# Optimization experiments

Measured on AMD Instinct MI355X. Metric: run time of the kernel, lower is better.

Reference implementation:

```python
import jax, jax.numpy as jnp
import numpy as np
import math

SIM_THRESHOLD = 0.05


def setup_inputs() -> dict:
    key = jax.random.key(0)
    ks = jax.random.split(key, 5)
    B, N, D = 32, 65, 512  # N = seq_len + 1
    gain = 1.0 / math.sqrt(2.0)
    lim = gain * math.sqrt(6.0 / (D + D))  # xavier_uniform with gain 1/sqrt(2)
    c = 1.0 / math.sqrt(D)
    return {
        "desc_embeddings": jax.random.normal(ks[0], (B, N - 1, D), jnp.float32),
        "name_value_embeddings": jax.random.normal(ks[1], (B, N, D), jnp.float32),
        "Wq": jax.random.uniform(ks[2], (D, D), jnp.float32, -lim, lim),
        "bq": jnp.zeros((D,), jnp.float32),
        "Wk": jax.random.uniform(ks[3], (D, D), jnp.float32, -lim, lim),
        "bk": jnp.zeros((D,), jnp.float32),
        "cls": jax.random.uniform(ks[4], (D,), jnp.float32, -c, c),
    }


def reference(desc_embeddings, name_value_embeddings, Wq, bq, Wk, bk, cls):
    # desc_embeddings is accepted but unused, exactly as in the torch module.
    nve = name_value_embeddings
    B, N, D = nve.shape
    S = N - 1

    q = nve @ Wq.T + bq  # [B, N, D]
    k = nve @ Wk.T + bk  # [B, N, D]
    attn = jnp.einsum('bid,bjd->bij', q, k) / math.sqrt(D)  # [B, N, N]

    # no_self_loop: multiplicatively zero the diagonal of the [1:,1:] block (pre-softmax)
    mask = jnp.ones((N, N), attn.dtype).at[1:, 1:].set(1.0 - jnp.eye(S, dtype=attn.dtype))
    attn = jax.nn.softmax(attn * mask, axis=-1)

    # row i's subgraph = {i} U {j : attn[b, i, j] > thr, j >= 1}
    members_all = (attn[:, 1:, 1:] > SIM_THRESHOLD) | jnp.eye(S, dtype=bool)  # [B, S, S]

    # Greedy sequential clustering: row i starts a subgraph only if node i is not
    # already used; its members then get marked used. Implemented with lax.scan
    # carrying the per-batch `used` bitmap (replaces the Python set loop).
    def step(used, xs):
        i, members = xs  # members: [B, S] for row i
        active = ~used[:, i]  # [B] -> is node (i+1) unused, i.e. this row is a leader
        sel = members & active[:, None]
        return used | sel, (active, sel)

    used0 = jnp.zeros((B, S), bool)
    _, (leader, member) = jax.lax.scan(
        step, used0, (jnp.arange(S), members_all.swapaxes(0, 1))
    )
    leader = leader.T.astype(nve.dtype)            # [B, S]
    member = member.transpose(1, 0, 2).astype(nve.dtype)  # [B, S, S]

    # Padded representation of the ragged output: for each leader row i,
    # slot 0 = cls token, slots 1..S = member embeddings (index order == sorted order),
    # zeros elsewhere. (out, leader_mask, member_mask) losslessly encode the
    # original list-of-lists of variable-size subgraphs.
    body = nve[:, None, 1:, :] * member[..., None]        # [B, S, S, D]
    cls_part = leader[:, :, None, None] * cls             # [B, S, 1, D]
    out = jnp.concatenate([cls_part, body], axis=2)       # [B, S, S+1, D]
    return out, leader, member
```

## Files before the change

### kernel.cpp

```cpp
#include <hip/hip_runtime.h>
#include <math.h>

constexpr int B = 32;
constexpr int N = 65;
constexpr int D = 512;
constexpr int S = 64;
constexpr int M = B * N;

constexpr size_t OUT0_ELEMS = (size_t)B * S * (S + 1) * D;
constexpr size_t Q_ELEMS    = (size_t)M * D;
constexpr size_t KT_ELEMS   = (size_t)B * D * N;
constexpr size_t STAGE_BASE = OUT0_ELEMS - Q_ELEMS - KT_ELEMS;
constexpr int ZF4 = (int)(STAGE_BASE / 4);

constexpr int NG_GEMM = 528;
constexpr int NG_FILL = 1536;
constexpr int NC = (B - 1) * S;
constexpr int NA = 1040;
constexpr int NB = 130;

__global__ __launch_bounds__(256) void k1_gemm_fill(
    const float* __restrict__ nve, const float* __restrict__ Wq,
    const float* __restrict__ bq, const float* __restrict__ Wk,
    const float* __restrict__ bk, float* __restrict__ out)
{
    __shared__ float As[32][68];
    __shared__ float Ws[32][68];

    const int gid = blockIdx.x;
    const int tid = threadIdx.x;

    if (gid < NG_GEMM) {
        const int mat = gid >= (NG_GEMM / 2);
        const int t   = mat ? gid - NG_GEMM / 2 : gid;
        const int bm  = (t % 33) * 64;
        const int bn  = (t / 33) * 64;
        const float* W    = mat ? Wk : Wq;
        const float* bias = mat ? bk : bq;

        float* q  = out + STAGE_BASE;
        float* kT = q + Q_ELEMS;

        const int tr = tid / 16;
        const int tc = tid % 16;
        float acc[4][4] = {};

        for (int k0 = 0; k0 < D; k0 += 32) {
            const int r  = tid / 8;
            const int c4 = (tid % 8) * 4;
            #pragma unroll
            for (int p = 0; p < 2; ++p) {
                const int rr = p * 32 + r;
                const int gm = bm + rr;
                float4 v = make_float4(0.f, 0.f, 0.f, 0.f);
                if (gm < M) v = *(const float4*)&nve[(size_t)gm * D + k0 + c4];
                As[c4 + 0][rr] = v.x; As[c4 + 1][rr] = v.y;
                As[c4 + 2][rr] = v.z; As[c4 + 3][rr] = v.w;
                float4 w = *(const float4*)&W[(size_t)(bn + rr) * D + k0 + c4];
                Ws[c4 + 0][rr] = w.x; Ws[c4 + 1][rr] = w.y;
                Ws[c4 + 2][rr] = w.z; Ws[c4 + 3][rr] = w.w;
            }
            __syncthreads();

            #pragma unroll
            for (int kk = 0; kk < 32; ++kk) {
                float a[4], w[4];
                #pragma unroll
                for (int u = 0; u < 4; ++u) a[u] = As[kk][tr * 4 + u];
                #pragma unroll
                for (int u = 0; u < 4; ++u) w[u] = Ws[kk][tc * 4 + u];
                #pragma unroll
                for (int i = 0; i < 4; ++i)
                    #pragma unroll
                    for (int j = 0; j < 4; ++j)
                        acc[i][j] += a[i] * w[j];
            }
            __syncthreads();
        }

        #pragma unroll
        for (int i = 0; i < 4; ++i) {
            const int gm = bm + tr * 4 + i;
            if (gm >= M) continue;
            const int b = gm / N;
            const int n = gm % N;
            if (mat == 0) {
                float4 v;
                v.x = acc[i][0] + bias[bn + tc * 4 + 0];
                v.y = acc[i][1] + bias[bn + tc * 4 + 1];
                v.z = acc[i][2] + bias[bn + tc * 4 + 2];
                v.w = acc[i][3] + bias[bn + tc * 4 + 3];
                *(float4*)&q[(size_t)gm * D + bn + tc * 4] = v;
            } else {
                #pragma unroll
                for (int j = 0; j < 4; ++j) {
                    const int gd = bn + tc * 4 + j;
                    kT[(size_t)b * D * N + (size_t)gd * N + n] = acc[i][j] + bias[gd];
                }
            }
        }
    } else {
        const float4 z = make_float4(0.f, 0.f, 0.f, 0.f);
        float4* o4 = (float4*)out;
        const int nthr = NG_FILL * 256;
        for (int f = (gid - NG_GEMM) * 256 + tid; f < ZF4; f += nthr)
            o4[f] = z;
    }
}

__global__ __launch_bounds__(128) void k2_attn(
    const float* __restrict__ out, unsigned long long* __restrict__ mem)
{
    const float* q  = out + STAGE_BASE;
    const float* kT = q + Q_ELEMS;

    const int bi = blockIdx.x;
    const int b = bi / S;
    const int r = bi % S;
    const int i = r + 1;
    const int t = threadIdx.x;

    __shared__ float qrow[D];
    __shared__ float sc[N];

    *(float4*)&qrow[t * 4] = *(const float4*)&q[((size_t)b * N + i) * D + t * 4];
    __syncthreads();

    if (t < N) {
        const float* kp = &kT[(size_t)b * D * N];
        float acc = 0.f;
        for (int e = 0; e < D; ++e) acc += qrow[e] * kp[(size_t)e * N + t];
        float s = acc * 0.044194173824159216f;
        if (t == i) s = 0.f;
        sc[t] = s;
    }
    __syncthreads();

    if (t < 64) {
        float mx = -INFINITY;
        for (int j = 0; j < N; ++j) mx = fmaxf(mx, sc[j]);
        float sum = 0.f;
        for (int j = 0; j < N; ++j) sum += expf(sc[j] - mx);
        const float p = expf(sc[t + 1] - mx) / sum;
        const bool bit = (p > 0.05f) || (t + 1 == i);
        unsigned long long mask = __ballot(bit);
        if (t == 0) mem[bi] = mask;
    }
}

__global__ void k3_cluster(const unsigned long long* __restrict__ mem,
                           unsigned long long* __restrict__ sel,
                           unsigned long long* __restrict__ lead)
{
    const int b = threadIdx.x;
    if (b >= B) return;
    unsigned long long used = 0ull, lb = 0ull;
    for (int i = 0; i < S; ++i) {
        const unsigned long long row = mem[b * S + i];
        const bool active = !((used >> i) & 1ull);
        const unsigned long long sl = active ? row : 0ull;
        used |= sl;
        lb |= (unsigned long long)active << i;
        sel[b * S + i] = sl;
    }
    lead[b] = lb;
}

__global__ __launch_bounds__(256) void k4_finish(
    const float* __restrict__ nve, const float* __restrict__ cls,
    const unsigned long long* __restrict__ sel,
    const unsigned long long* __restrict__ lead,
    float* __restrict__ out)
{
    const int gid = blockIdx.x;
    const int t = threadIdx.x;

    if (gid < NC) {
        const int b = gid / S;
        const int i = gid % S;
        const unsigned long long lb = lead[b];
        const unsigned long long sb = sel[b * S + i];
        const int h = t >> 7;
        const int tt = t & 127;
        float4* slot0 = (float4*)(out + (((size_t)b * S + i) * (S + 1)) * D);
        for (int s = h; s <= S; s += 2) {
            bool on = (s == 0) ? ((lb >> i) & 1ull) : ((sb >> (s - 1)) & 1ull);
            if (!on) continue;
            const float* src = (s == 0) ? cls : &nve[((size_t)b * N + s) * D];
            slot0[(size_t)s * 128 + tt] = ((const float4*)src)[tt];
        }
    } else if (gid < NC + NA) {
        const int ablk = gid - NC;
        const unsigned long long lb = lead[B - 1];
        float4* base4 = (float4*)out + STAGE_BASE / 4;
        #pragma unroll
        for (int u = 0; u < 2; ++u) {
            const int f = ablk * 512 + u * 256 + t;
            const int d4 = f & 127;
            const int slot = f >> 7;
            const int s = slot % (S + 1);
            const int i = slot / (S + 1);
            bool on;
            const float* src;
            if (s == 0) {
                on = (lb >> i) & 1ull;
                src = &cls[d4 * 4];
            } else {
                on = (sel[(B - 1) * S + i] >> (s - 1)) & 1ull;
                src = &nve[((size_t)(B - 1) * N + s) * D + d4 * 4];
            }
            float4 v = make_float4(0.f, 0.f, 0.f, 0.f);
            if (on) v = *(const float4*)src;
            base4[f] = v;
        }
    } else {
        const int f = (gid - NC - NA) * 256 + t;
        float* tail = out + OUT0_ELEMS;
        float4 v;
        #pragma unroll
        for (int c = 0; c < 4; ++c) {
            const int idx = f * 4 + c;
            float x;
            if (idx < B * S) {
                x = (float)((lead[idx / S] >> (idx % S)) & 1ull);
            } else {
                const int m = idx - B * S;
                const int b = m / (S * S);
                const int rem = m % (S * S);
                x = (float)((sel[b * S + rem / S] >> (rem % S)) & 1ull);
            }
            ((float*)&v)[c] = x;
        }
        *(float4*)&tail[(size_t)f * 4] = v;
    }
}

extern "C" void kernel_launch(void* const* d_in, const int* in_sizes, int n_in,
                              void* d_out, int out_size, void* d_ws, size_t ws_size,
                              hipStream_t stream) {
    const float* nve = (const float*)d_in[1];
    const float* Wq  = (const float*)d_in[2];
    const float* bq  = (const float*)d_in[3];
    const float* Wk  = (const float*)d_in[4];
    const float* bk  = (const float*)d_in[5];
    const float* cls = (const float*)d_in[6];

    float* out = (float*)d_out;

    unsigned long long* mem  = (unsigned long long*)d_ws;
    unsigned long long* sel  = mem + B * S;
    unsigned long long* lead = sel + B * S;

    k1_gemm_fill<<<NG_GEMM + NG_FILL, 256, 0, stream>>>(nve, Wq, bq, Wk, bk, out);
    k2_attn<<<B * S, 128, 0, stream>>>(out, mem);
    k3_cluster<<<1, 64, 0, stream>>>(mem, sel, lead);
    k4_finish<<<NC + NA + NB, 256, 0, stream>>>(nve, cls, sel, lead, out);
}
```

Measured before the change: 108.9 us.

## Spread output zero-fill across all kernels and batch four attention rows per block

The large zero-fill of the output buffer, previously done entirely in the first kernel, is now split across k1, k2 and k3, so the serial attention and clustering kernels also write zeros and keep memory bandwidth busy. The attention kernel computes four query rows per block so each key column load is reused four times. The finishing kernel now densely writes the remaining region, including staging space, for all batches rather than only the last batch. The hand-tuned split points (F_A, F_B, ROWS_SCATTER) must stay consistent with the staging buffer location, since later fills must not overwrite q/kT before k2 has read them.

```diff
diff --git a/kernel.cpp b/kernel.cpp
--- a/kernel.cpp
+++ b/kernel.cpp
@@ -11,13 +11,21 @@
 constexpr size_t Q_ELEMS    = (size_t)M * D;
 constexpr size_t KT_ELEMS   = (size_t)B * D * N;
 constexpr size_t STAGE_BASE = OUT0_ELEMS - Q_ELEMS - KT_ELEMS;
-constexpr int ZF4 = (int)(STAGE_BASE / 4);
+constexpr int OUT0_F4 = (int)(OUT0_ELEMS / 4);
+
+constexpr int F_A = 6291456;
+constexpr int F_B = 10485760;
+constexpr int ROW_F4 = (S + 1) * (D / 4);
+constexpr int ROWS_SCATTER = 1383;
+constexpr int F_C = ROW_F4 * ROWS_SCATTER;
 
 constexpr int NG_GEMM = 528;
 constexpr int NG_FILL = 1536;
-constexpr int NC = (B - 1) * S;
-constexpr int NA = 1040;
-constexpr int NB = 130;
+constexpr int N2_ATTN = 512;
+constexpr int N2_FILL = 768;
+constexpr int N3_FILL = 255;
+constexpr int N4_DENSE = 2048;
+constexpr int N4_TAIL  = 130;
 
 __global__ __launch_bounds__(256) void k1_gemm_fill(
     const float* __restrict__ nve, const float* __restrict__ Wq,
@@ -103,67 +111,108 @@
         const float4 z = make_float4(0.f, 0.f, 0.f, 0.f);
         float4* o4 = (float4*)out;
         const int nthr = NG_FILL * 256;
-        for (int f = (gid - NG_GEMM) * 256 + tid; f < ZF4; f += nthr)
+        for (int f = (gid - NG_GEMM) * 256 + tid; f < F_A; f += nthr)
             o4[f] = z;
     }
 }
 
-__global__ __launch_bounds__(128) void k2_attn(
-    const float* __restrict__ out, unsigned long long* __restrict__ mem)
+__global__ __launch_bounds__(256) void k2_attn(
+    const float* __restrict__ out, unsigned long long* __restrict__ mem,
+    float* __restrict__ outw)
 {
-    const float* q  = out + STAGE_BASE;
-    const float* kT = q + Q_ELEMS;
-
-    const int bi = blockIdx.x;
-    const int b = bi / S;
-    const int r = bi % S;
-    const int i = r + 1;
+    const int gid = blockIdx.x;
     const int t = threadIdx.x;
 
-    __shared__ float qrow[D];
-    __shared__ float sc[N];
-
-    *(float4*)&qrow[t * 4] = *(const float4*)&q[((size_t)b * N + i) * D + t * 4];
-    __syncthreads();
-
-    if (t < N) {
-        const float* kp = &kT[(size_t)b * D * N];
-        float acc = 0.f;
-        for (int e = 0; e < D; ++e) acc += qrow[e] * kp[(size_t)e * N + t];
-        float s = acc * 0.044194173824159216f;
-        if (t == i) s = 0.f;
-        sc[t] = s;
+    if (gid < N2_ATTN) {
+        const float* q  = out + STAGE_BASE;
+        const float* kT = q + Q_ELEMS;
+
+        const int b = gid / 16;
+        const int rbase = (gid % 16) * 4;
+
+        __shared__ float qrow[4][D];
+        __shared__ float sc[4][N];
+
+        #pragma unroll
+        for (int w = 0; w < 4; ++w) {
+            if (t < 128) {
+                const int i = rbase + w + 1;
+                *(float4*)&qrow[w][t * 4] =
+                    *(const float4*)&q[((size_t)b * N + i) * D + t * 4];
+            }
+        }
+        __syncthreads();
+
+        if (t < N) {
+            const float* kp = &kT[(size_t)b * D * N];
+            float a0 = 0.f, a1 = 0.f, a2 = 0.f, a3 = 0.f;
+            for (int e = 0; e < D; ++e) {
+                const float kv = kp[(size_t)e * N + t];
+                a0 += qrow[0][e] * kv;
+                a1 += qrow[1][e] * kv;
+                a2 += qrow[2][e] * kv;
+                a3 += qrow[3][e] * kv;
+            }
+            const float c = 0.044194173824159216f;
+            float s0 = a0 * c, s1 = a1 * c, s2 = a2 * c, s3 = a3 * c;
+            if (t == rbase + 1) s0 = 0.f;
+            if (t == rbase + 2) s1 = 0.f;
+            if (t == rbase + 3) s2 = 0.f;
+            if (t == rbase + 4) s3 = 0.f;
+            sc[0][t] = s0; sc[1][t] = s1; sc[2][t] = s2; sc[3][t] = s3;
+        }
+        __syncthreads();
+
+        {
+            const int w = t >> 6;
+            const int lane = t & 63;
+            const int i = rbase + w + 1;
+            float mx = -INFINITY;
+            for (int j = 0; j < N; ++j) mx = fmaxf(mx, sc[w][j]);
+            float sum = 0.f;
+            for (int j = 0; j < N; ++j) sum += expf(sc[w][j] - mx);
+            const float p = expf(sc[w][lane + 1] - mx) / sum;
+            const bool bit = (p > 0.05f) || (lane + 1 == i);
+            unsigned long long mask = __ballot(bit);
+            if (lane == 0) mem[b * S + rbase + w] = mask;
+        }
+    } else {
+        const float4 z = make_float4(0.f, 0.f, 0.f, 0.f);
+        float4* o4 = (float4*)outw;
+        const int nthr = N2_FILL * 256;
+        for (int f = F_A + (gid - N2_ATTN) * 256 + t; f < F_B; f += nthr)
+            o4[f] = z;
     }
-    __syncthreads();
-
-    if (t < 64) {
-        float mx = -INFINITY;
-        for (int j = 0; j < N; ++j) mx = fmaxf(mx, sc[j]);
-        float sum = 0.f;
-        for (int j = 0; j < N; ++j) sum += expf(sc[j] - mx);
-        const float p = expf(sc[t + 1] - mx) / sum;
-        const bool bit = (p > 0.05f) || (t + 1 == i);
-        unsigned long long mask = __ballot(bit);
-        if (t == 0) mem[bi] = mask;
+}
+
+__global__ __launch_bounds__(256) void k3_cluster(
+    const unsigned long long* __restrict__ mem,
+    unsigned long long* __restrict__ sel,
+    unsigned long long* __restrict__ lead,
+    float* __restrict__ out)
+{
+    const int gid = blockIdx.x;
+    const int t = threadIdx.x;
+    if (gid == 0) {
+        if (t >= B) return;
+        const int b = t;
+        unsigned long long used = 0ull, lb = 0ull;
+        for (int i = 0; i < S; ++i) {
+            const unsigned long long row = mem[b * S + i];
+            const bool active = !((used >> i) & 1ull);
+            const unsigned long long sl = active ? row : 0ull;
+            used |= sl;
+            lb |= (unsigned long long)active << i;
+            sel[b * S + i] = sl;
+        }
+        lead[b] = lb;
+    } else {
+        const float4 z = make_float4(0.f, 0.f, 0.f, 0.f);
+        float4* o4 = (float4*)out;
+        const int nthr = N3_FILL * 256;
+        for (int f = F_B + (gid - 1) * 256 + t; f < F_C; f += nthr)
+            o4[f] = z;
     }
-}
-
-__global__ void k3_cluster(const unsigned long long* __restrict__ mem,
-                           unsigned long long* __restrict__ sel,
-                           unsigned long long* __restrict__ lead)
-{
-    const int b = threadIdx.x;
-    if (b >= B) return;
-    unsigned long long used = 0ull, lb = 0ull;
-    for (int i = 0; i < S; ++i) {
-        const unsigned long long row = mem[b * S + i];
-        const bool active = !((used >> i) & 1ull);
-        const unsigned long long sl = active ? row : 0ull;
-        used |= sl;
-        lb |= (unsigned long long)active << i;
-        sel[b * S + i] = sl;
-    }
-    lead[b] = lb;
 }
 
 __global__ __launch_bounds__(256) void k4_finish(
@@ -175,7 +224,7 @@
     const int gid = blockIdx.x;
     const int t = threadIdx.x;
 
-    if (gid < NC) {
+    if (gid < ROWS_SCATTER) {
         const int b = gid / S;
         const int i = gid % S;
         const unsigned long long lb = lead[b];
@@ -189,32 +238,31 @@
             const float* src = (s == 0) ? cls : &nve[((size_t)b * N + s) * D];
             slot0[(size_t)s * 128 + tt] = ((const float4*)src)[tt];
         }
-    } else if (gid < NC + NA) {
-        const int ablk = gid - NC;
-        const unsigned long long lb = lead[B - 1];
-        float4* base4 = (float4*)out + STAGE_BASE / 4;
-        #pragma unroll
-        for (int u = 0; u < 2; ++u) {
-            const int f = ablk * 512 + u * 256 + t;
+    } else if (gid < ROWS_SCATTER + N4_DENSE) {
+        float4* o4 = (float4*)out;
+        const int nthr = N4_DENSE * 256;
+        for (int f = F_C + (gid - ROWS_SCATTER) * 256 + t; f < OUT0_F4; f += nthr) {
             const int d4 = f & 127;
             const int slot = f >> 7;
             const int s = slot % (S + 1);
-            const int i = slot / (S + 1);
+            const int row = slot / (S + 1);
+            const int i = row % S;
+            const int b = row / S;
             bool on;
             const float* src;
             if (s == 0) {
-                on = (lb >> i) & 1ull;
+                on = (lead[b] >> i) & 1ull;
                 src = &cls[d4 * 4];
             } else {
-                on = (sel[(B - 1) * S + i] >> (s - 1)) & 1ull;
-                src = &nve[((size_t)(B - 1) * N + s) * D + d4 * 4];
+                on = (sel[b * S + i] >> (s - 1)) & 1ull;
+                src = &nve[((size_t)b * N + s) * D + d4 * 4];
             }
             float4 v = make_float4(0.f, 0.f, 0.f, 0.f);
             if (on) v = *(const float4*)src;
-            base4[f] = v;
+            o4[f] = v;
         }
     } else {
-        const int f = (gid - NC - NA) * 256 + t;
+        const int f = (gid - ROWS_SCATTER - N4_DENSE) * 256 + t;
         float* tail = out + OUT0_ELEMS;
         float4 v;
         #pragma unroll
@@ -252,7 +300,7 @@
     unsigned long long* lead = sel + B * S;
 
     k1_gemm_fill<<<NG_GEMM + NG_FILL, 256, 0, stream>>>(nve, Wq, bq, Wk, bk, out);
-    k2_attn<<<B * S, 128, 0, stream>>>(out, mem);
-    k3_cluster<<<1, 64, 0, stream>>>(mem, sel, lead);
-    k4_finish<<<NC + NA + NB, 256, 0, stream>>>(nve, cls, sel, lead, out);
-}
+    k2_attn<<<N2_ATTN + N2_FILL, 256, 0, stream>>>(out, mem, out);
+    k3_cluster<<<1 + N3_FILL, 256, 0, stream>>>(mem, sel, lead, out);
+    k4_finish<<<ROWS_SCATTER + N4_DENSE + N4_TAIL, 256, 0, stream>>>(nve, cls, sel, lead, out);
+}
```

Result: slower. 116.5 us (+7.0%).

## Retile projection GEMM to 32x64 tiles with K-step 64 and more blocks

Applied to the files above, without the earlier changes.

The Q/K projection GEMM in the fused gemm+fill kernel moves from 64x64 output tiles with a 4x4 per-thread microtile and K-step 32 to 32x64 tiles with a 2x4 microtile and K-step 64, doubling the GEMM block count to 1040. Since M=2080 divides evenly by 32, the row bounds checks are dropped. The Ws reads become float4 and the bias is loaded as one float4. The goal is to spread the small GEMM over more CUs alongside the zero-fill blocks, accepting lower arithmetic intensity per thread and more redundant loads of W.

```diff
diff --git a/kernel.cpp b/kernel.cpp
--- a/kernel.cpp
+++ b/kernel.cpp
@@ -13,7 +13,7 @@
 constexpr size_t STAGE_BASE = OUT0_ELEMS - Q_ELEMS - KT_ELEMS;
 constexpr int ZF4 = (int)(STAGE_BASE / 4);
 
-constexpr int NG_GEMM = 528;
+constexpr int NG_GEMM = 1040;
 constexpr int NG_FILL = 1536;
 constexpr int NC = (B - 1) * S;
 constexpr int NA = 1040;
@@ -24,8 +24,8 @@
     const float* __restrict__ bq, const float* __restrict__ Wk,
     const float* __restrict__ bk, float* __restrict__ out)
 {
-    __shared__ float As[32][68];
-    __shared__ float Ws[32][68];
+    __shared__ float As[64][33];
+    __shared__ float Ws[64][68];
 
     const int gid = blockIdx.x;
     const int tid = threadIdx.x;
@@ -33,69 +33,76 @@
     if (gid < NG_GEMM) {
         const int mat = gid >= (NG_GEMM / 2);
         const int t   = mat ? gid - NG_GEMM / 2 : gid;
-        const int bm  = (t % 33) * 64;
-        const int bn  = (t / 33) * 64;
+        const int bm  = (t % 65) * 32;
+        const int bn  = (t / 65) * 64;
         const float* W    = mat ? Wk : Wq;
         const float* bias = mat ? bk : bq;
 
         float* q  = out + STAGE_BASE;
         float* kT = q + Q_ELEMS;
 
-        const int tr = tid / 16;
-        const int tc = tid % 16;
-        float acc[4][4] = {};
-
-        for (int k0 = 0; k0 < D; k0 += 32) {
-            const int r  = tid / 8;
-            const int c4 = (tid % 8) * 4;
+        const int tn4 = (tid & 15) * 4;
+        const int tm2 = (tid >> 4) * 2;
+
+        float4 acc0 = make_float4(0.f, 0.f, 0.f, 0.f);
+        float4 acc1 = make_float4(0.f, 0.f, 0.f, 0.f);
+
+        for (int k0 = 0; k0 < D; k0 += 64) {
             #pragma unroll
             for (int p = 0; p < 2; ++p) {
-                const int rr = p * 32 + r;
-                const int gm = bm + rr;
-                float4 v = make_float4(0.f, 0.f, 0.f, 0.f);
-                if (gm < M) v = *(const float4*)&nve[(size_t)gm * D + k0 + c4];
-                As[c4 + 0][rr] = v.x; As[c4 + 1][rr] = v.y;
-                As[c4 + 2][rr] = v.z; As[c4 + 3][rr] = v.w;
-                float4 w = *(const float4*)&W[(size_t)(bn + rr) * D + k0 + c4];
-                Ws[c4 + 0][rr] = w.x; Ws[c4 + 1][rr] = w.y;
-                Ws[c4 + 2][rr] = w.z; Ws[c4 + 3][rr] = w.w;
+                const int idx = p * 256 + tid;
+                const int row = idx >> 4;
+                const int c4  = (idx & 15) * 4;
+                const float4 v = *(const float4*)&nve[(size_t)(bm + row) * D + k0 + c4];
+                As[c4 + 0][row] = v.x; As[c4 + 1][row] = v.y;
+                As[c4 + 2][row] = v.z; As[c4 + 3][row] = v.w;
+            }
+            #pragma unroll
+            for (int p = 0; p < 4; ++p) {
+                const int idx = p * 256 + tid;
+                const int row = idx >> 4;
+                const int c4  = (idx & 15) * 4;
+                const float4 v = *(const float4*)&W[(size_t)(bn + row) * D + k0 + c4];
+                Ws[c4 + 0][row] = v.x; Ws[c4 + 1][row] = v.y;
+                Ws[c4 + 2][row] = v.z; Ws[c4 + 3][row] = v.w;
             }
             __syncthreads();
 
             #pragma unroll
-            for (int kk = 0; kk < 32; ++kk) {
-                float a[4], w[4];
-                #pragma unroll
-                for (int u = 0; u < 4; ++u) a[u] = As[kk][tr * 4 + u];
-                #pragma unroll
-                for (int u = 0; u < 4; ++u) w[u] = Ws[kk][tc * 4 + u];
-                #pragma unroll
-                for (int i = 0; i < 4; ++i)
-                    #pragma unroll
-                    for (int j = 0; j < 4; ++j)
-                        acc[i][j] += a[i] * w[j];
+            for (int kk = 0; kk < 64; ++kk) {
+                const float a0 = As[kk][tm2];
+                const float a1 = As[kk][tm2 + 1];
+                const float4 w = *(const float4*)&Ws[kk][tn4];
+                acc0.x += a0 * w.x; acc0.y += a0 * w.y;
+                acc0.z += a0 * w.z; acc0.w += a0 * w.w;
+                acc1.x += a1 * w.x; acc1.y += a1 * w.y;
+                acc1.z += a1 * w.z; acc1.w += a1 * w.w;
             }
             __syncthreads();
         }
 
-        #pragma unroll
-        for (int i = 0; i < 4; ++i) {
-            const int gm = bm + tr * 4 + i;
-            if (gm >= M) continue;
-            const int b = gm / N;
-            const int n = gm % N;
-            if (mat == 0) {
-                float4 v;
-                v.x = acc[i][0] + bias[bn + tc * 4 + 0];
-                v.y = acc[i][1] + bias[bn + tc * 4 + 1];
-                v.z = acc[i][2] + bias[bn + tc * 4 + 2];
-                v.w = acc[i][3] + bias[bn + tc * 4 + 3];
-                *(float4*)&q[(size_t)gm * D + bn + tc * 4] = v;
-            } else {
+        const int gm0 = bm + tm2;
+        const float4 b4 = *(const float4*)&bias[bn + tn4];
+        if (mat == 0) {
+            float4 r;
+            r.x = acc0.x + b4.x; r.y = acc0.y + b4.y;
+            r.z = acc0.z + b4.z; r.w = acc0.w + b4.w;
+            *(float4*)&q[(size_t)gm0 * D + bn + tn4] = r;
+            r.x = acc1.x + b4.x; r.y = acc1.y + b4.y;
+            r.z = acc1.z + b4.z; r.w = acc1.w + b4.w;
+            *(float4*)&q[(size_t)(gm0 + 1) * D + bn + tn4] = r;
+        } else {
+            #pragma unroll
+            for (int rr = 0; rr < 2; ++rr) {
+                const int gm = gm0 + rr;
+                const int b = gm / N;
+                const int n = gm % N;
+                const float* ac = rr ? (const float*)&acc1 : (const float*)&acc0;
+                const float* bi = (const float*)&b4;
                 #pragma unroll
                 for (int j = 0; j < 4; ++j) {
-                    const int gd = bn + tc * 4 + j;
-                    kT[(size_t)b * D * N + (size_t)gd * N + n] = acc[i][j] + bias[gd];
+                    const int gd = bn + tn4 + j;
+                    kT[(size_t)b * D * N + (size_t)gd * N + n] = ac[j] + bi[j];
                 }
             }
         }
```

Result: no change. 110.8 us (+1.8%).

## Deepen GEMM K-tile, vectorize LDS reads, batch attention rows per block

Applied to the files above, without the earlier changes.

The projection GEMM now stages 64-wide K slices instead of 32, which halves the number of sync rounds, and reads the shared-memory operands as float4. The attention kernel now handles 8 query rows per 256-thread block, with two rows per 64-lane wave, so each key load is reused across rows. Max and sum for the softmax are computed with wave shuffles instead of serial loops over shared memory. The larger LDS tile could lower occupancy, and the launch drops to 256 attention blocks, which fills fewer CUs.

```diff
diff --git a/kernel.cpp b/kernel.cpp
--- a/kernel.cpp
+++ b/kernel.cpp
@@ -15,6 +15,7 @@
 
 constexpr int NG_GEMM = 528;
 constexpr int NG_FILL = 1536;
+constexpr int N2_ATTN = 256;
 constexpr int NC = (B - 1) * S;
 constexpr int NA = 1040;
 constexpr int NB = 130;
@@ -24,8 +25,8 @@
     const float* __restrict__ bq, const float* __restrict__ Wk,
     const float* __restrict__ bk, float* __restrict__ out)
 {
-    __shared__ float As[32][68];
-    __shared__ float Ws[32][68];
+    __shared__ float As[64][68];
+    __shared__ float Ws[64][68];
 
     const int gid = blockIdx.x;
     const int tid = threadIdx.x;
@@ -45,57 +46,56 @@
         const int tc = tid % 16;
         float acc[4][4] = {};
 
-        for (int k0 = 0; k0 < D; k0 += 32) {
-            const int r  = tid / 8;
-            const int c4 = (tid % 8) * 4;
+        for (int k0 = 0; k0 < D; k0 += 64) {
             #pragma unroll
-            for (int p = 0; p < 2; ++p) {
-                const int rr = p * 32 + r;
-                const int gm = bm + rr;
+            for (int p = 0; p < 4; ++p) {
+                const int idx = p * 256 + tid;
+                const int row = idx >> 4;
+                const int c4  = (idx & 15) * 4;
+                const int gm = bm + row;
                 float4 v = make_float4(0.f, 0.f, 0.f, 0.f);
                 if (gm < M) v = *(const float4*)&nve[(size_t)gm * D + k0 + c4];
-                As[c4 + 0][rr] = v.x; As[c4 + 1][rr] = v.y;
-                As[c4 + 2][rr] = v.z; As[c4 + 3][rr] = v.w;
-                float4 w = *(const float4*)&W[(size_t)(bn + rr) * D + k0 + c4];
-                Ws[c4 + 0][rr] = w.x; Ws[c4 + 1][rr] = w.y;
-                Ws[c4 + 2][rr] = w.z; Ws[c4 + 3][rr] = w.w;
+                As[c4 + 0][row] = v.x; As[c4 + 1][row] = v.y;
+                As[c4 + 2][row] = v.z; As[c4 + 3][row] = v.w;
+                const float4 w = *(const float4*)&W[(size_t)(bn + row) * D + k0 + c4];
+                Ws[c4 + 0][row] = w.x; Ws[c4 + 1][row] = w.y;
+                Ws[c4 + 2][row] = w.z; Ws[c4 + 3][row] = w.w;
             }
             __syncthreads();
 
             #pragma unroll
-            for (int kk = 0; kk < 32; ++kk) {
-                float a[4], w[4];
-                #pragma unroll
-                for (int u = 0; u < 4; ++u) a[u] = As[kk][tr * 4 + u];
-                #pragma unroll
-                for (int u = 0; u < 4; ++u) w[u] = Ws[kk][tc * 4 + u];
+            for (int kk = 0; kk < 64; ++kk) {
+                const float4 a = *(const float4*)&As[kk][tr * 4];
+                const float4 w = *(const float4*)&Ws[kk][tc * 4];
+                const float* ap = (const float*)&a;
+                const float* wp = (const float*)&w;
                 #pragma unroll
                 for (int i = 0; i < 4; ++i)
                     #pragma unroll
                     for (int j = 0; j < 4; ++j)
-                        acc[i][j] += a[i] * w[j];
+                        acc[i][j] += ap[i] * wp[j];
             }
             __syncthreads();
         }
 
+        const float4 b4 = *(const float4*)&bias[bn + tc * 4];
+        const float* bp = (const float*)&b4;
         #pragma unroll
         for (int i = 0; i < 4; ++i) {
             const int gm = bm + tr * 4 + i;
             if (gm >= M) continue;
-            const int b = gm / N;
-            const int n = gm % N;
             if (mat == 0) {
                 float4 v;
-                v.x = acc[i][0] + bias[bn + tc * 4 + 0];
-                v.y = acc[i][1] + bias[bn + tc * 4 + 1];
-                v.z = acc[i][2] + bias[bn + tc * 4 + 2];
-                v.w = acc[i][3] + bias[bn + tc * 4 + 3];
+                v.x = acc[i][0] + bp[0]; v.y = acc[i][1] + bp[1];
+                v.z = acc[i][2] + bp[2]; v.w = acc[i][3] + bp[3];
                 *(float4*)&q[(size_t)gm * D + bn + tc * 4] = v;
             } else {
+                const int b = gm / N;
+                const int n = gm % N;
                 #pragma unroll
                 for (int j = 0; j < 4; ++j) {
                     const int gd = bn + tc * 4 + j;
-                    kT[(size_t)b * D * N + (size_t)gd * N + n] = acc[i][j] + bias[gd];
+                    kT[(size_t)b * D * N + (size_t)gd * N + n] = acc[i][j] + bp[j];
                 }
             }
         }
@@ -108,43 +108,66 @@
     }
 }
 
-__global__ __launch_bounds__(128) void k2_attn(
+__global__ __launch_bounds__(256) void k2_attn(
     const float* __restrict__ out, unsigned long long* __restrict__ mem)
 {
     const float* q  = out + STAGE_BASE;
     const float* kT = q + Q_ELEMS;
 
-    const int bi = blockIdx.x;
-    const int b = bi / S;
-    const int r = bi % S;
-    const int i = r + 1;
+    const int gid = blockIdx.x;
     const int t = threadIdx.x;
-
-    __shared__ float qrow[D];
-    __shared__ float sc[N];
-
-    *(float4*)&qrow[t * 4] = *(const float4*)&q[((size_t)b * N + i) * D + t * 4];
+    const int b  = gid >> 3;
+    const int r0 = (gid & 7) * 8;
+
+    __shared__ float qs[8][D];
+
+    #pragma unroll
+    for (int p = 0; p < 4; ++p) {
+        const int idx = p * 256 + t;
+        const int rl  = idx >> 7;
+        const int d4  = idx & 127;
+        const int i   = r0 + rl + 1;
+        *(float4*)&qs[rl][d4 * 4] =
+            *(const float4*)&q[((size_t)b * N + i) * D + d4 * 4];
+    }
     __syncthreads();
 
-    if (t < N) {
-        const float* kp = &kT[(size_t)b * D * N];
-        float acc = 0.f;
-        for (int e = 0; e < D; ++e) acc += qrow[e] * kp[(size_t)e * N + t];
-        float s = acc * 0.044194173824159216f;
-        if (t == i) s = 0.f;
-        sc[t] = s;
-    }
-    __syncthreads();
-
-    if (t < 64) {
-        float mx = -INFINITY;
-        for (int j = 0; j < N; ++j) mx = fmaxf(mx, sc[j]);
-        float sum = 0.f;
-        for (int j = 0; j < N; ++j) sum += expf(sc[j] - mx);
-        const float p = expf(sc[t + 1] - mx) / sum;
-        const bool bit = (p > 0.05f) || (t + 1 == i);
+    const int w = t >> 6;
+    const int l = t & 63;
+    const int rA = w * 2, rB = w * 2 + 1;
+    const int iA = r0 + rA + 1, iB = r0 + rB + 1;
+
+    const float* kp = &kT[(size_t)b * D * N];
+    float aA = 0.f, aB = 0.f, a0A = 0.f, a0B = 0.f;
+    #pragma unroll 4
+    for (int d = 0; d < D; ++d) {
+        const float kv0 = kp[d * N];
+        const float kv  = kp[d * N + 1 + l];
+        const float qa  = qs[rA][d];
+        const float qb  = qs[rB][d];
+        aA  += qa * kv;  aB  += qb * kv;
+        a0A += qa * kv0; a0B += qb * kv0;
+    }
+
+    const float c = 0.044194173824159216f;
+    #pragma unroll
+    for (int pass = 0; pass < 2; ++pass) {
+        const int i = pass ? iB : iA;
+        float s  = (pass ? aB : aA) * c;
+        const float s0 = (pass ? a0B : a0A) * c;
+        if (l == i - 1) s = 0.f;
+        float m = s;
+        #pragma unroll
+        for (int off = 32; off; off >>= 1) m = fmaxf(m, __shfl_xor(m, off));
+        m = fmaxf(m, s0);
+        float e = expf(s - m);
+        float sum = e;
+        #pragma unroll
+        for (int off = 32; off; off >>= 1) sum += __shfl_xor(sum, off);
+        sum += expf(s0 - m);
+        const bool bit = (e / sum > 0.05f) || (l == i - 1);
         unsigned long long mask = __ballot(bit);
-        if (t == 0) mem[bi] = mask;
+        if (l == 0) mem[b * S + i - 1] = mask;
     }
 }
 
@@ -252,7 +275,7 @@
     unsigned long long* lead = sel + B * S;
 
     k1_gemm_fill<<<NG_GEMM + NG_FILL, 256, 0, stream>>>(nve, Wq, bq, Wk, bk, out);
-    k2_attn<<<B * S, 128, 0, stream>>>(out, mem);
+    k2_attn<<<N2_ATTN, 256, 0, stream>>>(out, mem);
     k3_cluster<<<1, 64, 0, stream>>>(mem, sel, lead);
     k4_finish<<<NC + NA + NB, 256, 0, stream>>>(nve, cls, sel, lead, out);
 }
```

Result: slower. 137.4 us (+26.1%).
